# Kernel optimization log

Measured on AMD Instinct MI355X. Metric: run time of the kernel, lower is better.

The kernel has to match this reference:

```python
import jax, jax.numpy as jnp
import numpy as np

NUM_HEADS = 16


def setup_inputs() -> dict:
    key = jax.random.key(0)
    ks = jax.random.split(key, 8)
    B_, N, C = 2048, 64, 512
    nW = 64
    return {
        "x": jax.random.normal(ks[0], (B_, N, C), dtype=jnp.float32),
        "pe": jax.random.normal(ks[1], (1, N, C), dtype=jnp.float32),
        "rpe": jax.random.normal(ks[2], (NUM_HEADS, N, N), dtype=jnp.float32),
        "mask": jax.random.normal(ks[3], (nW, N, N), dtype=jnp.float32),
        "qkv_w": jax.random.normal(ks[4], (3 * C, C), dtype=jnp.float32) * 0.02,
        "qkv_b": jax.random.normal(ks[5], (3 * C,), dtype=jnp.float32) * 0.02,
        "proj_w": jax.random.normal(ks[6], (C, C), dtype=jnp.float32) * 0.02,
        "proj_b": jax.random.normal(ks[7], (C,), dtype=jnp.float32) * 0.02,
    }


def reference(x, pe, rpe, mask, qkv_w, qkv_b, proj_w, proj_b):
    B_, N, C = x.shape
    H = NUM_HEADS
    hd = C // H
    scale = hd ** -0.5
    xp = x + pe  # (B_, N, C)
    qkv = xp @ qkv_w.T + qkv_b  # (B_, N, 3C)
    qkv = qkv.reshape(B_, N, 3, H, hd).transpose(2, 0, 3, 1, 4)  # (3, B_, H, N, hd)
    q, k, v = qkv[0], qkv[1], qkv[2]
    attn = jnp.einsum("bhnd,bhmd->bhnm", q * scale, k)  # (B_, H, N, N)
    attn = attn + rpe[None]  # broadcast rpe over batch
    nW = mask.shape[0]
    attn = attn.reshape(B_ // nW, nW, H, N, N) + mask[None, :, None]
    attn = attn.reshape(B_, H, N, N)
    attn = jax.nn.softmax(attn, axis=-1)
    out = jnp.einsum("bhnm,bhmd->bhnd", attn, v)  # (B_, H, N, hd)
    out = out.transpose(0, 2, 1, 3).reshape(B_, N, C)
    return out @ proj_w.T + proj_b
```

## Files before the change

### kernel.cpp

```cpp
#include <hip/hip_runtime.h>
#include <hip/hip_bf16.h>
#include <cstdint>

typedef __bf16 bf16;
typedef __bf16 bf16x8_t __attribute__((ext_vector_type(8)));
typedef __bf16 bf16x4_t __attribute__((ext_vector_type(4)));
typedef float  f32x4_t  __attribute__((ext_vector_type(4)));

#define MFMA16(a, b, c) __builtin_amdgcn_mfma_f32_16x16x32_bf16((a), (b), (c), 0, 0, 0)

__device__ __forceinline__ void gload_lds16(const bf16* g, bf16* l) {
    __builtin_amdgcn_global_load_lds(
        (const __attribute__((address_space(1))) void*)g,
        (__attribute__((address_space(3))) void*)l,
        16, 0, 0);
}

__global__ void k_wprep(const float* __restrict__ wq, const float* __restrict__ wp,
                        bf16* __restrict__ wqb, bf16* __restrict__ wpb) {
    int t = blockIdx.x * 256 + threadIdx.x;
    int stride = gridDim.x * 256;
    for (int i = t; i < 196608; i += stride) {
        float4 v = ((const float4*)wq)[i];
        bf16x4_t o; o[0]=(bf16)v.x; o[1]=(bf16)v.y; o[2]=(bf16)v.z; o[3]=(bf16)v.w;
        ((bf16x4_t*)wqb)[i] = o;
    }
    for (int i = t; i < 65536; i += stride) {
        float4 v = ((const float4*)wp)[i];
        bf16x4_t o; o[0]=(bf16)v.x; o[1]=(bf16)v.y; o[2]=(bf16)v.z; o[3]=(bf16)v.w;
        ((bf16x4_t*)wpb)[i] = o;
    }
}

__device__ __forceinline__ void stage_ws(const bf16* __restrict__ wq, bf16* wsbuf,
                                         int h, int kt, int wave, int lane) {
#pragma unroll
    for (int ii = 0; ii < 3; ++ii) {
        int instr = wave * 3 + ii;
        int rr = instr * 4 + (lane >> 4);
        int s  = lane & 15;
        int gp = (s & 8) | ((s & 7) ^ (rr & 7));
        int R  = ((rr >> 5) << 9) + (h << 5) + (rr & 31);
        gload_lds16(wq + (size_t)R * 512 + kt * 128 + gp * 8, wsbuf + instr * 512);
    }
}

__global__ __launch_bounds__(512) void k_qkv_attn(
    const float* __restrict__ x,
    const float* __restrict__ pe,
    const float* __restrict__ rpe,
    const float* __restrict__ mask,
    const float* __restrict__ qkv_b,
    const bf16*  __restrict__ wq,
    bf16* __restrict__ ao)
{
    __shared__ bf16 Ws[2][96 * 128];
    __shared__ bf16 qs[2][64 * 40];
    __shared__ bf16 ks[2][64 * 40];
    __shared__ bf16 vts[2][32 * 72];
    __shared__ bf16 ps[2][64 * 72];

    const int tid  = threadIdx.x;
    const int lane = tid & 63;
    const int wave = tid >> 6;
    const int win  = wave >> 2;
    const int lr   = lane & 15;
    const int lg   = lane >> 4;
    const int row0 = (wave & 3) * 16;
    const int b2   = blockIdx.x * 2 + win;
    const int wi   = b2 & 63;

    bf16x8_t a[16];
    {
        const float* xr = x  + ((size_t)(b2 * 64 + row0 + lr)) * 512;
        const float* pr = pe + (size_t)(row0 + lr) * 512;
#pragma unroll
        for (int kc = 0; kc < 16; ++kc) {
            int k = kc * 32 + lg * 8;
            float4 x0 = *(const float4*)(xr + k);
            float4 x1 = *(const float4*)(xr + k + 4);
            float4 p0 = *(const float4*)(pr + k);
            float4 p1 = *(const float4*)(pr + k + 4);
            bf16x8_t v;
            v[0]=(bf16)(x0.x+p0.x); v[1]=(bf16)(x0.y+p0.y);
            v[2]=(bf16)(x0.z+p0.z); v[3]=(bf16)(x0.w+p0.w);
            v[4]=(bf16)(x1.x+p1.x); v[5]=(bf16)(x1.y+p1.y);
            v[6]=(bf16)(x1.z+p1.z); v[7]=(bf16)(x1.w+p1.w);
            a[kc] = v;
        }
    }

    const float SCALE = 0.17677669529663687f;

    stage_ws(wq, Ws[0], 0, 0, wave, lane);

    for (int h = 0; h < 16; ++h) {
        f32x4_t acc[6] = {};
#pragma unroll
        for (int kt = 0; kt < 4; ++kt) {
            const int ph = h * 4 + kt;
            if (ph < 63) {
                const int pn = ph + 1;
                stage_ws(wq, Ws[(kt + 1) & 1], pn >> 2, pn & 3, wave, lane);
                asm volatile("s_waitcnt vmcnt(3)" ::: "memory");
            } else {
                asm volatile("s_waitcnt vmcnt(0)" ::: "memory");
            }
            __builtin_amdgcn_s_barrier();
#pragma unroll
            for (int k2 = 0; k2 < 4; ++k2) {
                const int kc = kt * 4 + k2;
#pragma unroll
                for (int j = 0; j < 6; ++j) {
                    int row  = j * 16 + lr;
                    int p    = k2 * 4 + lg;
                    int phys = (p & 8) | ((p & 7) ^ (row & 7));
                    bf16x8_t bfrag = *(const bf16x8_t*)&Ws[kt & 1][row * 128 + phys * 8];
                    acc[j] = MFMA16(a[kc], bfrag, acc[j]);
                }
            }
            asm volatile("s_waitcnt lgkmcnt(0)" ::: "memory");
            __builtin_amdgcn_s_barrier();
        }

#pragma unroll
        for (int j = 0; j < 6; ++j) {
            int which = j >> 1;
            int colh  = (j & 1) * 16 + lr;
            float bj = qkv_b[which * 512 + h * 32 + colh];
#pragma unroll
            for (int r = 0; r < 4; ++r) {
                int row = row0 + lg * 4 + r;
                float val = acc[j][r] + bj;
                if (which == 0)      qs[win][row * 40 + colh] = (bf16)val;
                else if (which == 1) ks[win][row * 40 + colh] = (bf16)val;
                else                 vts[win][colh * 72 + row] = (bf16)val;
            }
        }
        asm volatile("s_waitcnt lgkmcnt(0)" ::: "memory");
        __builtin_amdgcn_s_barrier();

        const float* rp = rpe  + ((size_t)h)  * 4096;
        const float* mp = mask + ((size_t)wi) * 4096;
        float rm[4][4];
#pragma unroll
        for (int j = 0; j < 4; ++j) {
            int col = j * 16 + lr;
#pragma unroll
            for (int r = 0; r < 4; ++r) {
                int row = row0 + lg * 4 + r;
                rm[j][r] = rp[row * 64 + col] + mp[row * 64 + col];
            }
        }

        bf16x8_t aq = *(const bf16x8_t*)&qs[win][(row0 + lr) * 40 + lg * 8];
        f32x4_t s[4];
        f32x4_t zero = {};
#pragma unroll
        for (int j = 0; j < 4; ++j) {
            bf16x8_t bk = *(const bf16x8_t*)&ks[win][(j * 16 + lr) * 40 + lg * 8];
            s[j] = MFMA16(aq, bk, zero);
        }

        float mx[4] = {-1e30f, -1e30f, -1e30f, -1e30f};
#pragma unroll
        for (int j = 0; j < 4; ++j)
#pragma unroll
            for (int r = 0; r < 4; ++r) {
                float t = s[j][r] * SCALE + rm[j][r];
                s[j][r] = t;
                mx[r] = fmaxf(mx[r], t);
            }
#pragma unroll
        for (int r = 0; r < 4; ++r) {
            float m = mx[r];
            m = fmaxf(m, __shfl_xor(m, 1));
            m = fmaxf(m, __shfl_xor(m, 2));
            m = fmaxf(m, __shfl_xor(m, 4));
            m = fmaxf(m, __shfl_xor(m, 8));
            mx[r] = m;
        }
        float sm[4] = {0.f, 0.f, 0.f, 0.f};
#pragma unroll
        for (int j = 0; j < 4; ++j)
#pragma unroll
            for (int r = 0; r < 4; ++r) {
                float e = __expf(s[j][r] - mx[r]);
                s[j][r] = e;
                sm[r] += e;
            }
#pragma unroll
        for (int r = 0; r < 4; ++r) {
            float ssum = sm[r];
            ssum += __shfl_xor(ssum, 1);
            ssum += __shfl_xor(ssum, 2);
            ssum += __shfl_xor(ssum, 4);
            ssum += __shfl_xor(ssum, 8);
            sm[r] = 1.0f / ssum;
        }
#pragma unroll
        for (int j = 0; j < 4; ++j)
#pragma unroll
            for (int r = 0; r < 4; ++r)
                ps[win][(row0 + lg * 4 + r) * 72 + j * 16 + lr] = (bf16)s[j][r];

        f32x4_t o[2] = {};
#pragma unroll
        for (int kh = 0; kh < 2; ++kh) {
            bf16x8_t pa = *(const bf16x8_t*)&ps[win][(row0 + lr) * 72 + kh * 32 + lg * 8];
#pragma unroll
            for (int jd = 0; jd < 2; ++jd) {
                bf16x8_t bv = *(const bf16x8_t*)&vts[win][(jd * 16 + lr) * 72 + kh * 32 + lg * 8];
                o[jd] = MFMA16(pa, bv, o[jd]);
            }
        }
#pragma unroll
        for (int jd = 0; jd < 2; ++jd)
#pragma unroll
            for (int r = 0; r < 4; ++r) {
                int row = row0 + lg * 4 + r;
                ao[((size_t)(b2 * 64 + row)) * 512 + h * 32 + jd * 16 + lr] =
                    (bf16)(o[jd][r] * sm[r]);
            }
    }
}

__global__ __launch_bounds__(256) void k_proj(
    const bf16* __restrict__ A, const bf16* __restrict__ Bw,
    const float* __restrict__ bias, float* __restrict__ C)
{
    __shared__ bf16 As[128 * 72];
    __shared__ bf16 Bs[128 * 72];

    const int tid  = threadIdx.x;
    const int lane = tid & 63;
    const int wave = tid >> 6;
    const int lr = lane & 15, lg = lane >> 4;
    const int wr = wave >> 1, wc = wave & 1;
    const int bid = blockIdx.x;
    const int wg  = (bid & 7) * 512 + (bid >> 3);
    const int mb = wg >> 2, nb = wg & 3;
    const size_t m0 = (size_t)mb * 128;
    const int n0 = nb * 128;

    f32x4_t acc[4][4] = {};

    for (int kt = 0; kt < 8; ++kt) {
        const int k0 = kt * 64;
        bf16x8_t va[4], vb[4];
#pragma unroll
        for (int j = 0; j < 4; ++j) {
            int c = tid + 256 * j;
            int row = c >> 3, i8 = (c & 7) * 8;
            va[j] = *(const bf16x8_t*)(A  + (m0 + row) * 512 + k0 + i8);
            vb[j] = *(const bf16x8_t*)(Bw + (size_t)(n0 + row) * 512 + k0 + i8);
        }
        __syncthreads();
#pragma unroll
        for (int j = 0; j < 4; ++j) {
            int c = tid + 256 * j;
            int row = c >> 3, i8 = (c & 7) * 8;
            *(bf16x8_t*)&As[row * 72 + i8] = va[j];
            *(bf16x8_t*)&Bs[row * 72 + i8] = vb[j];
        }
        __syncthreads();

#pragma unroll
        for (int k2 = 0; k2 < 2; ++k2) {
            bf16x8_t af[4], bfr[4];
#pragma unroll
            for (int i = 0; i < 4; ++i)
                af[i] = *(const bf16x8_t*)&As[(wr * 64 + i * 16 + lr) * 72 + k2 * 32 + lg * 8];
#pragma unroll
            for (int j = 0; j < 4; ++j)
                bfr[j] = *(const bf16x8_t*)&Bs[(wc * 64 + j * 16 + lr) * 72 + k2 * 32 + lg * 8];
#pragma unroll
            for (int i = 0; i < 4; ++i)
#pragma unroll
                for (int j = 0; j < 4; ++j)
                    acc[i][j] = MFMA16(af[i], bfr[j], acc[i][j]);
        }
    }

    float bj[4];
#pragma unroll
    for (int j = 0; j < 4; ++j) bj[j] = bias[n0 + wc * 64 + j * 16 + lr];
#pragma unroll
    for (int i = 0; i < 4; ++i) {
#pragma unroll
        for (int j = 0; j < 4; ++j) {
            int col = n0 + wc * 64 + j * 16 + lr;
#pragma unroll
            for (int r = 0; r < 4; ++r) {
                size_t row = m0 + wr * 64 + i * 16 + lg * 4 + r;
                C[row * 512 + col] = acc[i][j][r] + bj[j];
            }
        }
    }
}

extern "C" void kernel_launch(void* const* d_in, const int* in_sizes, int n_in,
                              void* d_out, int out_size, void* d_ws, size_t ws_size,
                              hipStream_t stream) {
    (void)in_sizes; (void)n_in; (void)out_size; (void)ws_size;
    const float* x      = (const float*)d_in[0];
    const float* pe     = (const float*)d_in[1];
    const float* rpe    = (const float*)d_in[2];
    const float* mask   = (const float*)d_in[3];
    const float* qkv_w  = (const float*)d_in[4];
    const float* qkv_b  = (const float*)d_in[5];
    const float* proj_w = (const float*)d_in[6];
    const float* proj_b = (const float*)d_in[7];
    float* out = (float*)d_out;

    char* ws = (char*)d_ws;
    bf16* wqkvb  = (bf16*)ws;
    bf16* wprojb = (bf16*)(ws + 1572864);
    bf16* ao     = (bf16*)(ws + 2097152);

    k_wprep<<<256, 256, 0, stream>>>(qkv_w, proj_w, wqkvb, wprojb);
    k_qkv_attn<<<1024, 512, 0, stream>>>(x, pe, rpe, mask, qkv_b, wqkvb, ao);
    k_proj<<<4096, 256, 0, stream>>>(ao, wprojb, proj_b, out);
}
```

Baseline: 675.1 us.

## Process four windows per block with 32 rows per wave to reuse weight tiles

Each block now handles four attention windows instead of two, and each wave computes 32 rows (two MFMA row tiles) in place of 16. Every weight fragment read from LDS feeds two MFMAs, halving weight staging traffic per window, and the grid shrinks to 512 blocks. The cost is doubled register use for activations and accumulators (a[2][16], acc[2][6]), which may lower occupancy or cause spills. LDS for q/k/v/p buffers also doubles. The qkv bias loads are hoisted ahead of the GEMM loop.

```diff
diff --git a/kernel.cpp b/kernel.cpp
--- a/kernel.cpp
+++ b/kernel.cpp
@@ -55,25 +55,27 @@
     bf16* __restrict__ ao)
 {
     __shared__ bf16 Ws[2][96 * 128];
-    __shared__ bf16 qs[2][64 * 40];
-    __shared__ bf16 ks[2][64 * 40];
-    __shared__ bf16 vts[2][32 * 72];
-    __shared__ bf16 ps[2][64 * 72];
+    __shared__ bf16 qs[4][64 * 40];
+    __shared__ bf16 ks[4][64 * 40];
+    __shared__ bf16 vts[4][32 * 72];
+    __shared__ bf16 ps[4][64 * 72];
 
     const int tid  = threadIdx.x;
     const int lane = tid & 63;
     const int wave = tid >> 6;
-    const int win  = wave >> 2;
+    const int win  = wave >> 1;
+    const int half = wave & 1;
     const int lr   = lane & 15;
     const int lg   = lane >> 4;
-    const int row0 = (wave & 3) * 16;
-    const int b2   = blockIdx.x * 2 + win;
-    const int wi   = b2 & 63;
-
-    bf16x8_t a[16];
-    {
-        const float* xr = x  + ((size_t)(b2 * 64 + row0 + lr)) * 512;
-        const float* pr = pe + (size_t)(row0 + lr) * 512;
+    const int row0 = half * 32;
+    const int b4   = blockIdx.x * 4 + win;
+    const int wi   = b4 & 63;
+
+    bf16x8_t a[2][16];
+#pragma unroll
+    for (int t = 0; t < 2; ++t) {
+        const float* xr = x  + ((size_t)(b4 * 64 + row0 + t * 16 + lr)) * 512;
+        const float* pr = pe + (size_t)(row0 + t * 16 + lr) * 512;
 #pragma unroll
         for (int kc = 0; kc < 16; ++kc) {
             int k = kc * 32 + lg * 8;
@@ -86,7 +88,7 @@
             v[2]=(bf16)(x0.z+p0.z); v[3]=(bf16)(x0.w+p0.w);
             v[4]=(bf16)(x1.x+p1.x); v[5]=(bf16)(x1.y+p1.y);
             v[6]=(bf16)(x1.z+p1.z); v[7]=(bf16)(x1.w+p1.w);
-            a[kc] = v;
+            a[t][kc] = v;
         }
     }
 
@@ -95,7 +97,12 @@
     stage_ws(wq, Ws[0], 0, 0, wave, lane);
 
     for (int h = 0; h < 16; ++h) {
-        f32x4_t acc[6] = {};
+        float bpre[6];
+#pragma unroll
+        for (int j = 0; j < 6; ++j)
+            bpre[j] = qkv_b[(j >> 1) * 512 + h * 32 + (j & 1) * 16 + lr];
+
+        f32x4_t acc[2][6] = {};
 #pragma unroll
         for (int kt = 0; kt < 4; ++kt) {
             const int ph = h * 4 + kt;
@@ -116,7 +123,8 @@
                     int p    = k2 * 4 + lg;
                     int phys = (p & 8) | ((p & 7) ^ (row & 7));
                     bf16x8_t bfrag = *(const bf16x8_t*)&Ws[kt & 1][row * 128 + phys * 8];
-                    acc[j] = MFMA16(a[kc], bfrag, acc[j]);
+                    acc[0][j] = MFMA16(a[0][kc], bfrag, acc[0][j]);
+                    acc[1][j] = MFMA16(a[1][kc], bfrag, acc[1][j]);
                 }
             }
             asm volatile("s_waitcnt lgkmcnt(0)" ::: "memory");
@@ -124,104 +132,107 @@
         }
 
 #pragma unroll
-        for (int j = 0; j < 6; ++j) {
-            int which = j >> 1;
-            int colh  = (j & 1) * 16 + lr;
-            float bj = qkv_b[which * 512 + h * 32 + colh];
-#pragma unroll
-            for (int r = 0; r < 4; ++r) {
-                int row = row0 + lg * 4 + r;
-                float val = acc[j][r] + bj;
-                if (which == 0)      qs[win][row * 40 + colh] = (bf16)val;
-                else if (which == 1) ks[win][row * 40 + colh] = (bf16)val;
-                else                 vts[win][colh * 72 + row] = (bf16)val;
-            }
-        }
+        for (int t = 0; t < 2; ++t)
+#pragma unroll
+            for (int j = 0; j < 6; ++j) {
+                int which = j >> 1;
+                int colh  = (j & 1) * 16 + lr;
+#pragma unroll
+                for (int r = 0; r < 4; ++r) {
+                    int row = row0 + t * 16 + lg * 4 + r;
+                    float val = acc[t][j][r] + bpre[j];
+                    if (which == 0)      qs[win][row * 40 + colh] = (bf16)val;
+                    else if (which == 1) ks[win][row * 40 + colh] = (bf16)val;
+                    else                 vts[win][colh * 72 + row] = (bf16)val;
+                }
+            }
         asm volatile("s_waitcnt lgkmcnt(0)" ::: "memory");
         __builtin_amdgcn_s_barrier();
 
         const float* rp = rpe  + ((size_t)h)  * 4096;
         const float* mp = mask + ((size_t)wi) * 4096;
-        float rm[4][4];
-#pragma unroll
-        for (int j = 0; j < 4; ++j) {
-            int col = j * 16 + lr;
+
+#pragma unroll
+        for (int t = 0; t < 2; ++t) {
+            bf16x8_t aq = *(const bf16x8_t*)&qs[win][(row0 + t * 16 + lr) * 40 + lg * 8];
+            f32x4_t s[4];
+            f32x4_t zero = {};
+#pragma unroll
+            for (int j = 0; j < 4; ++j) {
+                bf16x8_t bk = *(const bf16x8_t*)&ks[win][(j * 16 + lr) * 40 + lg * 8];
+                s[j] = MFMA16(aq, bk, zero);
+            }
+            float rm[4][4];
+#pragma unroll
+            for (int j = 0; j < 4; ++j) {
+                int col = j * 16 + lr;
+#pragma unroll
+                for (int r = 0; r < 4; ++r) {
+                    int row = row0 + t * 16 + lg * 4 + r;
+                    rm[j][r] = rp[row * 64 + col] + mp[row * 64 + col];
+                }
+            }
+            float mx[4] = {-1e30f, -1e30f, -1e30f, -1e30f};
+#pragma unroll
+            for (int j = 0; j < 4; ++j)
+#pragma unroll
+                for (int r = 0; r < 4; ++r) {
+                    float tv = s[j][r] * SCALE + rm[j][r];
+                    s[j][r] = tv;
+                    mx[r] = fmaxf(mx[r], tv);
+                }
 #pragma unroll
             for (int r = 0; r < 4; ++r) {
-                int row = row0 + lg * 4 + r;
-                rm[j][r] = rp[row * 64 + col] + mp[row * 64 + col];
-            }
-        }
-
-        bf16x8_t aq = *(const bf16x8_t*)&qs[win][(row0 + lr) * 40 + lg * 8];
-        f32x4_t s[4];
-        f32x4_t zero = {};
-#pragma unroll
-        for (int j = 0; j < 4; ++j) {
-            bf16x8_t bk = *(const bf16x8_t*)&ks[win][(j * 16 + lr) * 40 + lg * 8];
-            s[j] = MFMA16(aq, bk, zero);
-        }
-
-        float mx[4] = {-1e30f, -1e30f, -1e30f, -1e30f};
-#pragma unroll
-        for (int j = 0; j < 4; ++j)
+                float m = mx[r];
+                m = fmaxf(m, __shfl_xor(m, 1));
+                m = fmaxf(m, __shfl_xor(m, 2));
+                m = fmaxf(m, __shfl_xor(m, 4));
+                m = fmaxf(m, __shfl_xor(m, 8));
+                mx[r] = m;
+            }
+            float sm[4] = {0.f, 0.f, 0.f, 0.f};
+#pragma unroll
+            for (int j = 0; j < 4; ++j)
+#pragma unroll
+                for (int r = 0; r < 4; ++r) {
+                    float e = __expf(s[j][r] - mx[r]);
+                    s[j][r] = e;
+                    sm[r] += e;
+                }
 #pragma unroll
             for (int r = 0; r < 4; ++r) {
-                float t = s[j][r] * SCALE + rm[j][r];
-                s[j][r] = t;
-                mx[r] = fmaxf(mx[r], t);
-            }
-#pragma unroll
-        for (int r = 0; r < 4; ++r) {
-            float m = mx[r];
-            m = fmaxf(m, __shfl_xor(m, 1));
-            m = fmaxf(m, __shfl_xor(m, 2));
-            m = fmaxf(m, __shfl_xor(m, 4));
-            m = fmaxf(m, __shfl_xor(m, 8));
-            mx[r] = m;
-        }
-        float sm[4] = {0.f, 0.f, 0.f, 0.f};
-#pragma unroll
-        for (int j = 0; j < 4; ++j)
-#pragma unroll
-            for (int r = 0; r < 4; ++r) {
-                float e = __expf(s[j][r] - mx[r]);
-                s[j][r] = e;
-                sm[r] += e;
-            }
-#pragma unroll
-        for (int r = 0; r < 4; ++r) {
-            float ssum = sm[r];
-            ssum += __shfl_xor(ssum, 1);
-            ssum += __shfl_xor(ssum, 2);
-            ssum += __shfl_xor(ssum, 4);
-            ssum += __shfl_xor(ssum, 8);
-            sm[r] = 1.0f / ssum;
-        }
-#pragma unroll
-        for (int j = 0; j < 4; ++j)
-#pragma unroll
-            for (int r = 0; r < 4; ++r)
-                ps[win][(row0 + lg * 4 + r) * 72 + j * 16 + lr] = (bf16)s[j][r];
-
-        f32x4_t o[2] = {};
-#pragma unroll
-        for (int kh = 0; kh < 2; ++kh) {
-            bf16x8_t pa = *(const bf16x8_t*)&ps[win][(row0 + lr) * 72 + kh * 32 + lg * 8];
-#pragma unroll
-            for (int jd = 0; jd < 2; ++jd) {
-                bf16x8_t bv = *(const bf16x8_t*)&vts[win][(jd * 16 + lr) * 72 + kh * 32 + lg * 8];
-                o[jd] = MFMA16(pa, bv, o[jd]);
-            }
-        }
-#pragma unroll
-        for (int jd = 0; jd < 2; ++jd)
-#pragma unroll
-            for (int r = 0; r < 4; ++r) {
-                int row = row0 + lg * 4 + r;
-                ao[((size_t)(b2 * 64 + row)) * 512 + h * 32 + jd * 16 + lr] =
-                    (bf16)(o[jd][r] * sm[r]);
-            }
+                float ssum = sm[r];
+                ssum += __shfl_xor(ssum, 1);
+                ssum += __shfl_xor(ssum, 2);
+                ssum += __shfl_xor(ssum, 4);
+                ssum += __shfl_xor(ssum, 8);
+                sm[r] = 1.0f / ssum;
+            }
+#pragma unroll
+            for (int j = 0; j < 4; ++j)
+#pragma unroll
+                for (int r = 0; r < 4; ++r)
+                    ps[win][(row0 + t * 16 + lg * 4 + r) * 72 + j * 16 + lr] = (bf16)s[j][r];
+
+            f32x4_t o[2] = {};
+#pragma unroll
+            for (int kh = 0; kh < 2; ++kh) {
+                bf16x8_t pa = *(const bf16x8_t*)&ps[win][(row0 + t * 16 + lr) * 72 + kh * 32 + lg * 8];
+#pragma unroll
+                for (int jd = 0; jd < 2; ++jd) {
+                    bf16x8_t bv = *(const bf16x8_t*)&vts[win][(jd * 16 + lr) * 72 + kh * 32 + lg * 8];
+                    o[jd] = MFMA16(pa, bv, o[jd]);
+                }
+            }
+#pragma unroll
+            for (int jd = 0; jd < 2; ++jd)
+#pragma unroll
+                for (int r = 0; r < 4; ++r) {
+                    int row = row0 + t * 16 + lg * 4 + r;
+                    ao[((size_t)(b4 * 64 + row)) * 512 + h * 32 + jd * 16 + lr] =
+                        (bf16)(o[jd][r] * sm[r]);
+                }
+        }
     }
 }
 
@@ -319,6 +330,6 @@
     bf16* ao     = (bf16*)(ws + 2097152);
 
     k_wprep<<<256, 256, 0, stream>>>(qkv_w, proj_w, wqkvb, wprojb);
-    k_qkv_attn<<<1024, 512, 0, stream>>>(x, pe, rpe, mask, qkv_b, wqkvb, ao);
+    k_qkv_attn<<<512, 512, 0, stream>>>(x, pe, rpe, mask, qkv_b, wqkvb, ao);
     k_proj<<<4096, 256, 0, stream>>>(ao, wprojb, proj_b, out);
 }
```

Measured after the change: 779.8 us. +15.5%, slower.
